# Kernel optimization log

Hardware: AMD Instinct MI355X
Metric: run time of the kernel (lower is better)

Reference implementation:

```python
import jax, jax.numpy as jnp
import numpy as np

B, T, NE = 2, 2048, 1024
NH, NKV, HD = 16, 4, 64
GC = 32  # ve_gate_channels
WIN = 1024  # sliding window (left)
EPS = 1e-6


def rope(x, cos, sin):
    # x: (B,T,H,D), cos/sin: (B,T,D//2)
    cos = cos[:, :, None, :]
    sin = sin[:, :, None, :]
    x1, x2 = jnp.split(x, 2, axis=-1)
    return jnp.concatenate([x1 * cos + x2 * sin, -x1 * sin + x2 * cos], axis=-1)


def rmsnorm(x):
    return x * jax.lax.rsqrt(jnp.mean(x * x, axis=-1, keepdims=True) + EPS)


def setup_inputs() -> dict:
    key = jax.random.key(0)
    ks = jax.random.split(key, 7)
    x = jax.random.normal(ks[0], (B, T, NE), jnp.float32)
    ve = jax.random.normal(ks[1], (B, T, NKV * HD), jnp.float32)
    # real RoPE tables (already 'sliced to correct positions')
    inv_freq = 1.0 / (10000.0 ** (jnp.arange(HD // 2, dtype=jnp.float32) / (HD // 2)))
    ang = jnp.arange(T, dtype=jnp.float32)[:, None] * inv_freq[None, :]  # (T, D//2)
    cos = jnp.broadcast_to(jnp.cos(ang)[None], (B, T, HD // 2))
    sin = jnp.broadcast_to(jnp.sin(ang)[None], (B, T, HD // 2))
    s = 0.02
    Wq = jax.random.normal(ks[2], (NE, NH * HD), jnp.float32) * s
    Wk = jax.random.normal(ks[3], (NE, NKV * HD), jnp.float32) * s
    Wv = jax.random.normal(ks[4], (NE, NKV * HD), jnp.float32) * s
    Wo = jax.random.normal(ks[5], (NE, NE), jnp.float32) * s
    Wg = jax.random.normal(ks[6], (GC, NKV), jnp.float32) * s
    return {"x": x, "ve": ve, "cos": cos, "sin": sin,
            "Wq": Wq, "Wk": Wk, "Wv": Wv, "Wo": Wo, "Wg": Wg,
            "window_size": WIN}


def reference(x, ve, cos, sin, Wq, Wk, Wv, Wo, Wg, window_size):
    Bs, Ts, _ = x.shape
    q = (x @ Wq).reshape(Bs, Ts, NH, HD)
    k = (x @ Wk).reshape(Bs, Ts, NKV, HD)
    v = (x @ Wv).reshape(Bs, Ts, NKV, HD)
    # gated value embeddings
    gate = 2.0 * jax.nn.sigmoid(x[..., :GC] @ Wg)  # (B,T,NKV)
    v = v + gate[..., None] * ve.reshape(Bs, Ts, NKV, HD)
    q = rmsnorm(rope(q, cos, sin))
    k = rmsnorm(rope(k, cos, sin))
    # GQA: head h uses kv head h // rep
    rep = NH // NKV
    k = jnp.repeat(k, rep, axis=2)
    v = jnp.repeat(v, rep, axis=2)
    scale = 1.0 / jnp.sqrt(jnp.float32(HD))
    scores = jnp.einsum('bthd,bshd->bhts', q, k) * scale  # (B,H,T,T)
    i = jnp.arange(Ts)[:, None]
    j = jnp.arange(Ts)[None, :]
    mask = (j <= i) & (i - j <= window_size)  # causal + sliding window
    scores = jnp.where(mask, scores, -jnp.inf)
    p = jax.nn.softmax(scores, axis=-1)
    y = jnp.einsum('bhts,bshd->bthd', p, v).reshape(Bs, Ts, NE)
    return y @ Wo
```

## Files before the change

kernel.cpp:

```cpp
#include <hip/hip_runtime.h>
#include <hip/hip_bf16.h>
#include <string.h>

typedef __attribute__((ext_vector_type(8))) short bf16x8;
typedef __attribute__((ext_vector_type(4))) short bf16x4;
typedef __attribute__((ext_vector_type(4))) float f32x4;
typedef __attribute__((ext_vector_type(4))) int i32x4;
typedef __attribute__((ext_vector_type(2))) int i32x2;

#define DEV __device__ __forceinline__
#define WIN_ 1024

DEV short f2bf(float f) {
  __hip_bfloat16 h = __float2bfloat16(f);
  short s; __builtin_memcpy(&s, &h, 2); return s;
}
DEV float bf2f(short s) {
  union { unsigned u; float f; } a; a.u = ((unsigned)(unsigned short)s) << 16;
  return a.f;
}
DEV unsigned pkbf2(float a, float b) {
  __hip_bfloat162 h = __float22bfloat162_rn(make_float2(a, b));
  unsigned u; __builtin_memcpy(&u, &h, 4); return u;
}
DEV float fexp2(float x) {
#if __has_builtin(__builtin_amdgcn_exp2f)
  return __builtin_amdgcn_exp2f(x);
#else
  return exp2f(x);
#endif
}

DEV f32x4 mfma16(bf16x4 a, bf16x4 b, f32x4 c) {
#if __has_builtin(__builtin_amdgcn_mfma_f32_16x16x16bf16_1k)
  return __builtin_amdgcn_mfma_f32_16x16x16bf16_1k(a, b, c, 0, 0, 0);
#else
  asm volatile("s_nop 1\n\tv_mfma_f32_16x16x16_bf16 %0, %1, %2, %0\n\ts_nop 7\n\ts_nop 7"
               : "+v"(c) : "v"(a), "v"(b));
  return c;
#endif
}

DEV void gload16(const short* g, short* l) {
  __builtin_amdgcn_global_load_lds((const __attribute__((address_space(1))) unsigned int*)g,
                                   (__attribute__((address_space(3))) unsigned int*)l,
                                   16, 0, 0);
}

__global__ __launch_bounds__(256) void k_prep(const float* __restrict__ x,
    const float* __restrict__ Wq, const float* __restrict__ Wk, const float* __restrict__ Wv,
    const float* __restrict__ Wo, short* __restrict__ xb, short* __restrict__ WbT,
    short* __restrict__ WoT) {
  const int bid = blockIdx.x;
  if (bid < 4096) {
    int i = bid * 256 + threadIdx.x;
    f32x4 v = *(const f32x4*)(x + (size_t)i * 4);
    i32x2 o = {(int)pkbf2(v[0], v[1]), (int)pkbf2(v[2], v[3])};
    *(i32x2*)(xb + (size_t)i * 4) = o;
    return;
  }
  int t = bid - 4096;
  const float* src; short* dst; int srcld, bx, by;
  if (t < 1024)      { src = Wq; dst = WbT;                        srcld = 1024; bx = t & 31;          by = t >> 5; }
  else if (t < 1280) { src = Wk; dst = WbT + (size_t)1024 * 1024;  srcld = 256;  bx = (t - 1024) & 7;  by = (t - 1024) >> 3; }
  else if (t < 1536) { src = Wv; dst = WbT + (size_t)1280 * 1024;  srcld = 256;  bx = (t - 1280) & 7;  by = (t - 1280) >> 3; }
  else               { src = Wo; dst = WoT;                        srcld = 1024; bx = (t - 1536) & 31; by = (t - 1536) >> 5; }
  __shared__ float tile[32][33];
  const int n0 = bx * 32, k0 = by * 32;
  const int tx = threadIdx.x & 31, ty = threadIdx.x >> 5;
#pragma unroll
  for (int i = 0; i < 4; ++i)
    tile[ty * 4 + i][tx] = src[(size_t)(k0 + ty * 4 + i) * srcld + n0 + tx];
  __syncthreads();
#pragma unroll
  for (int i = 0; i < 4; ++i)
    dst[(size_t)(n0 + ty * 4 + i) * 1024 + k0 + tx] = f2bf(tile[tx][ty * 4 + i]);
}

__global__ __launch_bounds__(256) void k_gemm_qkv(const short* __restrict__ A, const short* __restrict__ BT,
    const float* __restrict__ x, const float* __restrict__ ve,
    const float* __restrict__ cosp, const float* __restrict__ sinp, const float* __restrict__ Wg,
    short* __restrict__ qh, short* __restrict__ kh, short* __restrict__ vhT) {
  const int K = 1024;
  __shared__ short As[2][8192];
  __shared__ short Bs[2][4096];
  const int tid = threadIdx.x;
  const int l = tid & 63, w = tid >> 6;
  const int l15 = l & 15, hi = l >> 4;
  const int bx = blockIdx.x;
  const int m0 = blockIdx.y * 128, n0 = bx * 64;
  const int srow = tid >> 3;
  const int segsw = 8 * ((tid & 7) ^ (srow & 7));
  const int lo = tid * 8;
  const short* pa = A + (size_t)(m0 + srow) * K + segsw;
  const short* pb = BT + (size_t)(n0 + srow) * K + segsw;
  const int f8 = l15 & 7;

  f32x4 acc[2][4];
#pragma unroll
  for (int i = 0; i < 2; ++i)
#pragma unroll
    for (int j = 0; j < 4; ++j) acc[i][j] = (f32x4){0.f, 0.f, 0.f, 0.f};

  auto stage = [&](int buf, int koff) {
    gload16(pa + koff,          &As[buf][lo]);
    gload16(pa + 32 * K + koff, &As[buf][lo + 2048]);
    gload16(pa + 64 * K + koff, &As[buf][lo + 4096]);
    gload16(pa + 96 * K + koff, &As[buf][lo + 6144]);
    gload16(pb + koff,          &Bs[buf][lo]);
    gload16(pb + 32 * K + koff, &Bs[buf][lo + 2048]);
  };

  stage(0, 0);
  __syncthreads();
  int cur = 0;
  for (int k0 = 0; k0 < K; k0 += 64) {
    if (k0 + 64 < K) stage(cur ^ 1, k0 + 64);
    bf16x8 af[2][2], bfr[4][2];
#pragma unroll
    for (int c = 0; c < 2; ++c) {
      int seg = 8 * ((4 * c + hi) ^ f8);
#pragma unroll
      for (int mi = 0; mi < 2; ++mi)
        af[mi][c] = *(const bf16x8*)&As[cur][(32 * w + 16 * mi + l15) * 64 + seg];
#pragma unroll
      for (int ni = 0; ni < 4; ++ni)
        bfr[ni][c] = *(const bf16x8*)&Bs[cur][(16 * ni + l15) * 64 + seg];
    }
#pragma unroll
    for (int c = 0; c < 2; ++c)
#pragma unroll
      for (int mi = 0; mi < 2; ++mi)
#pragma unroll
        for (int ni = 0; ni < 4; ++ni)
          acc[mi][ni] = __builtin_amdgcn_mfma_f32_16x16x32_bf16(af[mi][c], bfr[ni][c], acc[mi][ni], 0, 0, 0);
    __syncthreads();
    cur ^= 1;
  }

  if (bx < 20) {
    short* dst0 = (bx < 16) ? qh : kh;
#pragma unroll
    for (int mi = 0; mi < 2; ++mi)
#pragma unroll
      for (int r = 0; r < 4; ++r) {
        int bt = m0 + 32 * w + 16 * mi + 4 * hi + r;
        int b = bt >> 11, t = bt & 2047;
        float c0 = cosp[bt * 32 + l15],      s0 = sinp[bt * 32 + l15];
        float c1 = cosp[bt * 32 + 16 + l15], s1 = sinp[bt * 32 + 16 + l15];
        float a0 = acc[mi][0][r], b0 = acc[mi][2][r];
        float a1 = acc[mi][1][r], b1 = acc[mi][3][r];
        float o0 = a0 * c0 + b0 * s0;
        float o2 = b0 * c0 - a0 * s0;
        float o1 = a1 * c1 + b1 * s1;
        float o3 = b1 * c1 - a1 * s1;
        float ss = o0 * o0 + o1 * o1 + o2 * o2 + o3 * o3;
        ss += __shfl_xor(ss, 1); ss += __shfl_xor(ss, 2);
        ss += __shfl_xor(ss, 4); ss += __shfl_xor(ss, 8);
        float rinv = rsqrtf(ss * (1.f / 64.f) + 1e-6f);
        if (bx < 16) rinv *= 0.18033688011112042f;
        size_t rb = ((size_t)((b * ((bx < 16) ? 16 : 4) + ((bx < 16) ? bx : bx - 16)) * 2048 + t)) * 64;
        dst0[rb + l15]      = f2bf(o0 * rinv);
        dst0[rb + 16 + l15] = f2bf(o1 * rinv);
        dst0[rb + 32 + l15] = f2bf(o2 * rinv);
        dst0[rb + 48 + l15] = f2bf(o3 * rinv);
      }
  } else {
    const int kvh = bx - 20;
#pragma unroll
    for (int mi = 0; mi < 2; ++mi)
#pragma unroll
      for (int r = 0; r < 4; ++r) {
        int bt = m0 + 32 * w + 16 * mi + 4 * hi + r;
        int b = bt >> 11, t = bt & 2047;
        const float* xr = x + (size_t)bt * 1024;
        float z = 0.f;
#pragma unroll
        for (int gg = 0; gg < 32; ++gg) z += xr[gg] * Wg[gg * 4 + kvh];
        float gate = 2.f / (1.f + __expf(-z));
        const float* vep = ve + (size_t)bt * 256 + kvh * 64;
        short* dst = vhT + (size_t)(b * 4 + kvh) * 131072 + t;
#pragma unroll
        for (int ni = 0; ni < 4; ++ni) {
          int d = 16 * ni + l15;
          float vv = acc[mi][ni][r] + gate * vep[d];
          dst[(size_t)d * 2048] = f2bf(vv);
        }
      }
  }
}

template <int LDC, bool F32OUT>
__global__ __launch_bounds__(256) void k_gemm_bt(const short* __restrict__ A, const short* __restrict__ BT,
                                                 void* __restrict__ Cv, int K) {
  __shared__ short As[2][8192];
  __shared__ short Bs[2][4096];
  const int tid = threadIdx.x;
  const int l = tid & 63, w = tid >> 6;
  const int l15 = l & 15, hi = l >> 4;
  const int m0 = blockIdx.y * 128, n0 = blockIdx.x * 64;
  const int srow = tid >> 3;
  const int segsw = 8 * ((tid & 7) ^ (srow & 7));
  const int lo = tid * 8;
  const short* pa = A + (size_t)(m0 + srow) * K + segsw;
  const short* pb = BT + (size_t)(n0 + srow) * K + segsw;
  const int f8 = l15 & 7;

  f32x4 acc[2][4];
#pragma unroll
  for (int i = 0; i < 2; ++i)
#pragma unroll
    for (int j = 0; j < 4; ++j) acc[i][j] = (f32x4){0.f, 0.f, 0.f, 0.f};

  auto stage = [&](int buf, int koff) {
    gload16(pa + koff,          &As[buf][lo]);
    gload16(pa + 32 * K + koff, &As[buf][lo + 2048]);
    gload16(pa + 64 * K + koff, &As[buf][lo + 4096]);
    gload16(pa + 96 * K + koff, &As[buf][lo + 6144]);
    gload16(pb + koff,          &Bs[buf][lo]);
    gload16(pb + 32 * K + koff, &Bs[buf][lo + 2048]);
  };

  stage(0, 0);
  __syncthreads();
  int cur = 0;
  for (int k0 = 0; k0 < K; k0 += 64) {
    if (k0 + 64 < K) stage(cur ^ 1, k0 + 64);
    bf16x8 af[2][2], bfr[4][2];
#pragma unroll
    for (int c = 0; c < 2; ++c) {
      int seg = 8 * ((4 * c + hi) ^ f8);
#pragma unroll
      for (int mi = 0; mi < 2; ++mi)
        af[mi][c] = *(const bf16x8*)&As[cur][(32 * w + 16 * mi + l15) * 64 + seg];
#pragma unroll
      for (int ni = 0; ni < 4; ++ni)
        bfr[ni][c] = *(const bf16x8*)&Bs[cur][(16 * ni + l15) * 64 + seg];
    }
#pragma unroll
    for (int c = 0; c < 2; ++c)
#pragma unroll
      for (int mi = 0; mi < 2; ++mi)
#pragma unroll
        for (int ni = 0; ni < 4; ++ni)
          acc[mi][ni] = __builtin_amdgcn_mfma_f32_16x16x32_bf16(af[mi][c], bfr[ni][c], acc[mi][ni], 0, 0, 0);
    __syncthreads();
    cur ^= 1;
  }
#pragma unroll
  for (int mi = 0; mi < 2; ++mi)
#pragma unroll
    for (int ni = 0; ni < 4; ++ni)
#pragma unroll
      for (int r = 0; r < 4; ++r) {
        int crow = m0 + 32 * w + 16 * mi + 4 * hi + r;
        int ccol = n0 + 16 * ni + l15;
        if (F32OUT) ((float*)Cv)[(size_t)crow * LDC + ccol] = acc[mi][ni][r];
        else        ((short*)Cv)[(size_t)crow * LDC + ccol] = f2bf(acc[mi][ni][r]);
      }
}

__global__ __launch_bounds__(256) void k_attn(const short* __restrict__ qh, const short* __restrict__ kh,
                                              const short* __restrict__ vhT, short* __restrict__ yb) {
  __shared__ i32x4 lds4[2][1024];
  char* base = (char*)lds4;
  const int bid = blockIdx.x;
  const int kq = bid >> 8, low = bid & 255;
  const int h = low & 15, b = (low >> 4) & 1, q0 = low >> 5;
  const int qt = (kq == 0) ? (31 - q0) : (kq == 1) ? (16 + q0) : (kq == 2) ? (15 - q0) : q0;
  const int kvh = h >> 2;
  const int qs = qt * 64;
  const int tid = threadIdx.x;
  const int w = tid >> 6, l = tid & 63, l15 = l & 15, hi = l >> 4;
  const int qi = qs + 16 * w + l15;
  const int rsw = (l15 & 7) << 4;

  const short* qb = qh + ((size_t)((b * 16 + h) * 2048 + qs + 16 * w + l15)) * 64;
  bf16x8 qf0 = *(const bf16x8*)(qb + 8 * hi);
  bf16x8 qf1 = *(const bf16x8*)(qb + 32 + 8 * hi);

  f32x4 oacc[4];
#pragma unroll
  for (int i = 0; i < 4; ++i) oacc[i] = (f32x4){0.f, 0.f, 0.f, 0.f};
  float lsum = 0.f;

  const int kt_lo = (qs >= 1024) ? ((qs - 1024) >> 6) : 0;
  const int kt_hi = qs >> 6;
  const short* kbase = kh + ((size_t)(b * 4 + kvh) * 2048) * 64;
  const short* vbase = vhT + ((size_t)(b * 4 + kvh) * 64) * 2048;

  const int srow = tid >> 3, sseg = tid & 7;
  const int swz = (srow & 7) << 4;
  const int ko = ((srow << 7) + (sseg << 4)) ^ swz;
  const short* kp = kbase + (size_t)(kt_lo * 64 + srow) * 64 + sseg * 8;
  const short* vp = vbase + (size_t)srow * 2048 + kt_lo * 64 + sseg * 8;
  i32x4 rk0, rk1, rv0, rv1;

#define LOADT() do { \
    rk0 = *(const i32x4*)kp; \
    rk1 = *(const i32x4*)(kp + 2048); \
    rv0 = *(const i32x4*)vp; \
    rv1 = *(const i32x4*)(vp + 32 * 2048); \
  } while (0)

#define WRITET(DST) do { \
    char* kd = (DST); \
    *(i32x4*)(kd + ko) = rk0; \
    *(i32x4*)(kd + ko + 4096) = rk1; \
    char* vd = kd + 8192; \
    *(i32x4*)(vd + ko) = rv0; \
    *(i32x4*)(vd + ko + 4096) = rv1; \
  } while (0)

  auto TILE = [&](char* kbuf, int kt) {
    char* vbuf = kbuf + 8192;
    f32x4 s[4];
#pragma unroll
    for (int nt = 0; nt < 4; ++nt) s[nt] = (f32x4){0.f, 0.f, 0.f, 0.f};
#pragma unroll
    for (int c = 0; c < 2; ++c) {
      bf16x8 qc = c ? qf1 : qf0;
#pragma unroll
      for (int nt = 0; nt < 4; ++nt) {
        bf16x8 kf = *(const bf16x8*)(kbuf + ((((16 * nt + l15) << 7) + (c << 6) + (hi << 4)) ^ rsw));
        s[nt] = __builtin_amdgcn_mfma_f32_16x16x32_bf16(kf, qc, s[nt], 0, 0, 0);
      }
    }
    if (kt == kt_lo || kt == kt_hi) {
      const int k0 = kt * 64;
#pragma unroll
      for (int nt = 0; nt < 4; ++nt)
#pragma unroll
        for (int r = 0; r < 4; ++r) {
          int kj = k0 + 16 * nt + 4 * hi + r;
          if (kj > qi || (qi - kj) > WIN_) s[nt][r] = -1e30f;
        }
    }
#pragma unroll
    for (int nt = 0; nt < 4; ++nt)
#pragma unroll
      for (int r = 0; r < 4; ++r) s[nt][r] = fexp2(fminf(s[nt][r], 12.5f));
    float r0 = (s[0][0] + s[0][1]) + (s[0][2] + s[0][3]);
    float r1 = (s[1][0] + s[1][1]) + (s[1][2] + s[1][3]);
    float r2 = (s[2][0] + s[2][1]) + (s[2][2] + s[2][3]);
    float r3 = (s[3][0] + s[3][1]) + (s[3][2] + s[3][3]);
    lsum += (r0 + r1) + (r2 + r3);

    bf16x4 pa[4];
#pragma unroll
    for (int nt = 0; nt < 4; ++nt) {
      i32x2 pk = {(int)pkbf2(s[nt][0], s[nt][1]), (int)pkbf2(s[nt][2], s[nt][3])};
      pa[nt] = __builtin_bit_cast(bf16x4, pk);
    }
#pragma unroll
    for (int dt = 0; dt < 4; ++dt) {
      int rowb = ((16 * dt + l15) << 7) + (hi << 3);
#pragma unroll
      for (int nt = 0; nt < 4; ++nt) {
        i32x2 vv = *(const i32x2*)(vbuf + ((rowb + 32 * nt) ^ rsw));
        oacc[dt] = mfma16(__builtin_bit_cast(bf16x4, vv), pa[nt], oacc[dt]);
      }
    }
  };

  LOADT();
  WRITET(base);
  __syncthreads();

  int kt = kt_lo;
  for (;;) {
    if (kt < kt_hi) { kp += 4096; vp += 64; LOADT(); }
    __builtin_amdgcn_s_setprio(1);
    TILE(base, kt);
    __builtin_amdgcn_s_setprio(0);
    if (kt < kt_hi) WRITET(base + 16384);
    __syncthreads();
    if (kt == kt_hi) break;
    ++kt;
    if (kt < kt_hi) { kp += 4096; vp += 64; LOADT(); }
    __builtin_amdgcn_s_setprio(1);
    TILE(base + 16384, kt);
    __builtin_amdgcn_s_setprio(0);
    if (kt < kt_hi) WRITET(base);
    __syncthreads();
    if (kt == kt_hi) break;
    ++kt;
  }
#undef LOADT
#undef WRITET

  lsum += __shfl_xor(lsum, 16);
  lsum += __shfl_xor(lsum, 32);

  float inv = 1.f / lsum;
  size_t orow = (size_t)(b * 2048 + qs + 16 * w + l15);
#pragma unroll
  for (int dt = 0; dt < 4; ++dt) {
    int col0 = h * 64 + 16 * dt + 4 * hi;
    i32x2 pk = {(int)pkbf2(oacc[dt][0] * inv, oacc[dt][1] * inv),
                (int)pkbf2(oacc[dt][2] * inv, oacc[dt][3] * inv)};
    *(i32x2*)(yb + orow * 1024 + col0) = pk;
  }
}

extern "C" void kernel_launch(void* const* d_in, const int* in_sizes, int n_in,
                              void* d_out, int out_size, void* d_ws, size_t ws_size,
                              hipStream_t stream) {
  const float* x    = (const float*)d_in[0];
  const float* ve   = (const float*)d_in[1];
  const float* cosp = (const float*)d_in[2];
  const float* sinp = (const float*)d_in[3];
  const float* Wq   = (const float*)d_in[4];
  const float* Wk   = (const float*)d_in[5];
  const float* Wv   = (const float*)d_in[6];
  const float* Wo   = (const float*)d_in[7];
  const float* Wg   = (const float*)d_in[8];
  float* out = (float*)d_out;

  char* ws = (char*)d_ws;
  short* xb   = (short*)(ws);
  short* WbT  = (short*)(ws + 8388608);
  short* WoT  = (short*)(ws + 11534336);
  short* qh   = (short*)(ws + 26214400);
  short* kh   = (short*)(ws + 34603008);
  short* vhT  = (short*)(ws + 36700160);
  short* yb   = (short*)(ws + 38797312);

  k_prep<<<6656, 256, 0, stream>>>(x, Wq, Wk, Wv, Wo, xb, WbT, WoT);

  k_gemm_qkv<<<dim3(24, 32), 256, 0, stream>>>(xb, WbT, x, ve, cosp, sinp, Wg, qh, kh, vhT);

  k_attn<<<1024, 256, 0, stream>>>(qh, kh, vhT, yb);

  k_gemm_bt<1024, true><<<dim3(16, 32), 256, 0, stream>>>(yb, WoT, out, 1024);
}
```

Baseline: 85.77 us.

## Fuse x fp32-to-bf16 conversion into QKV GEMM A-tile staging; narrow attn setprio

The separate pass converting x to bf16 in the prep kernel is removed. The QKV GEMM now loads fp32 x directly into registers, packs it to bf16, and writes it to LDS after the MFMA loop, with prefetching done through registers instead of async global-to-LDS copies. This drops one full write and read of the bf16 copy of x and shrinks the prep launch. The cost is that each GEMM block rereads fp32 x, doing twice the A bytes per tile across 24 column blocks, and uses more registers. Attention setprio regions are also narrowed to cover only the MFMA sections.

```diff
diff --git a/kernel.cpp b/kernel.cpp
--- a/kernel.cpp
+++ b/kernel.cpp
@@ -47,19 +47,10 @@
                                    16, 0, 0);
 }
 
-__global__ __launch_bounds__(256) void k_prep(const float* __restrict__ x,
-    const float* __restrict__ Wq, const float* __restrict__ Wk, const float* __restrict__ Wv,
-    const float* __restrict__ Wo, short* __restrict__ xb, short* __restrict__ WbT,
-    short* __restrict__ WoT) {
-  const int bid = blockIdx.x;
-  if (bid < 4096) {
-    int i = bid * 256 + threadIdx.x;
-    f32x4 v = *(const f32x4*)(x + (size_t)i * 4);
-    i32x2 o = {(int)pkbf2(v[0], v[1]), (int)pkbf2(v[2], v[3])};
-    *(i32x2*)(xb + (size_t)i * 4) = o;
-    return;
-  }
-  int t = bid - 4096;
+__global__ __launch_bounds__(256) void k_prep(const float* __restrict__ Wq, const float* __restrict__ Wk,
+    const float* __restrict__ Wv, const float* __restrict__ Wo,
+    short* __restrict__ WbT, short* __restrict__ WoT) {
+  int t = blockIdx.x;
   const float* src; short* dst; int srcld, bx, by;
   if (t < 1024)      { src = Wq; dst = WbT;                        srcld = 1024; bx = t & 31;          by = t >> 5; }
   else if (t < 1280) { src = Wk; dst = WbT + (size_t)1024 * 1024;  srcld = 256;  bx = (t - 1024) & 7;  by = (t - 1024) >> 3; }
@@ -77,7 +68,7 @@
     dst[(size_t)(n0 + ty * 4 + i) * 1024 + k0 + tx] = f2bf(tile[tx][ty * 4 + i]);
 }
 
-__global__ __launch_bounds__(256) void k_gemm_qkv(const short* __restrict__ A, const short* __restrict__ BT,
+__global__ __launch_bounds__(256) void k_gemm_qkv(const short* __restrict__ BT,
     const float* __restrict__ x, const float* __restrict__ ve,
     const float* __restrict__ cosp, const float* __restrict__ sinp, const float* __restrict__ Wg,
     short* __restrict__ qh, short* __restrict__ kh, short* __restrict__ vhT) {
@@ -92,7 +83,7 @@
   const int srow = tid >> 3;
   const int segsw = 8 * ((tid & 7) ^ (srow & 7));
   const int lo = tid * 8;
-  const short* pa = A + (size_t)(m0 + srow) * K + segsw;
+  const float* pxa = x + (size_t)(m0 + srow) * 1024 + segsw;
   const short* pb = BT + (size_t)(n0 + srow) * K + segsw;
   const int f8 = l15 & 7;
 
@@ -102,20 +93,37 @@
 #pragma unroll
     for (int j = 0; j < 4; ++j) acc[i][j] = (f32x4){0.f, 0.f, 0.f, 0.f};
 
-  auto stage = [&](int buf, int koff) {
-    gload16(pa + koff,          &As[buf][lo]);
-    gload16(pa + 32 * K + koff, &As[buf][lo + 2048]);
-    gload16(pa + 64 * K + koff, &As[buf][lo + 4096]);
-    gload16(pa + 96 * K + koff, &As[buf][lo + 6144]);
+  f32x4 u[8];
+  auto stage_load = [&](int koff) {
+#pragma unroll
+    for (int ch = 0; ch < 4; ++ch) {
+      const float* p = pxa + (size_t)ch * 32768 + koff;
+      u[2 * ch]     = *(const f32x4*)p;
+      u[2 * ch + 1] = *(const f32x4*)(p + 4);
+    }
+  };
+  auto stage_write = [&](int buf) {
+#pragma unroll
+    for (int ch = 0; ch < 4; ++ch) {
+      i32x4 pk = {(int)pkbf2(u[2 * ch][0], u[2 * ch][1]),
+                  (int)pkbf2(u[2 * ch][2], u[2 * ch][3]),
+                  (int)pkbf2(u[2 * ch + 1][0], u[2 * ch + 1][1]),
+                  (int)pkbf2(u[2 * ch + 1][2], u[2 * ch + 1][3])};
+      *(i32x4*)&As[buf][lo + ch * 2048] = pk;
+    }
+  };
+  auto stage_b = [&](int buf, int koff) {
     gload16(pb + koff,          &Bs[buf][lo]);
     gload16(pb + 32 * K + koff, &Bs[buf][lo + 2048]);
   };
 
-  stage(0, 0);
+  stage_load(0);
+  stage_b(0, 0);
+  stage_write(0);
   __syncthreads();
   int cur = 0;
   for (int k0 = 0; k0 < K; k0 += 64) {
-    if (k0 + 64 < K) stage(cur ^ 1, k0 + 64);
+    if (k0 + 64 < K) { stage_load(k0 + 64); stage_b(cur ^ 1, k0 + 64); }
     bf16x8 af[2][2], bfr[4][2];
 #pragma unroll
     for (int c = 0; c < 2; ++c) {
@@ -134,6 +142,7 @@
 #pragma unroll
         for (int ni = 0; ni < 4; ++ni)
           acc[mi][ni] = __builtin_amdgcn_mfma_f32_16x16x32_bf16(af[mi][c], bfr[ni][c], acc[mi][ni], 0, 0, 0);
+    if (k0 + 64 < K) stage_write(cur ^ 1);
     __syncthreads();
     cur ^= 1;
   }
@@ -317,6 +326,7 @@
     f32x4 s[4];
 #pragma unroll
     for (int nt = 0; nt < 4; ++nt) s[nt] = (f32x4){0.f, 0.f, 0.f, 0.f};
+    __builtin_amdgcn_s_setprio(1);
 #pragma unroll
     for (int c = 0; c < 2; ++c) {
       bf16x8 qc = c ? qf1 : qf0;
@@ -326,6 +336,7 @@
         s[nt] = __builtin_amdgcn_mfma_f32_16x16x32_bf16(kf, qc, s[nt], 0, 0, 0);
       }
     }
+    __builtin_amdgcn_s_setprio(0);
     if (kt == kt_lo || kt == kt_hi) {
       const int k0 = kt * 64;
 #pragma unroll
@@ -352,6 +363,7 @@
       i32x2 pk = {(int)pkbf2(s[nt][0], s[nt][1]), (int)pkbf2(s[nt][2], s[nt][3])};
       pa[nt] = __builtin_bit_cast(bf16x4, pk);
     }
+    __builtin_amdgcn_s_setprio(1);
 #pragma unroll
     for (int dt = 0; dt < 4; ++dt) {
       int rowb = ((16 * dt + l15) << 7) + (hi << 3);
@@ -361,6 +373,7 @@
         oacc[dt] = mfma16(__builtin_bit_cast(bf16x4, vv), pa[nt], oacc[dt]);
       }
     }
+    __builtin_amdgcn_s_setprio(0);
   };
 
   LOADT();
@@ -370,17 +383,13 @@
   int kt = kt_lo;
   for (;;) {
     if (kt < kt_hi) { kp += 4096; vp += 64; LOADT(); }
-    __builtin_amdgcn_s_setprio(1);
     TILE(base, kt);
-    __builtin_amdgcn_s_setprio(0);
     if (kt < kt_hi) WRITET(base + 16384);
     __syncthreads();
     if (kt == kt_hi) break;
     ++kt;
     if (kt < kt_hi) { kp += 4096; vp += 64; LOADT(); }
-    __builtin_amdgcn_s_setprio(1);
     TILE(base + 16384, kt);
-    __builtin_amdgcn_s_setprio(0);
     if (kt < kt_hi) WRITET(base);
     __syncthreads();
     if (kt == kt_hi) break;
@@ -418,7 +427,6 @@
   float* out = (float*)d_out;
 
   char* ws = (char*)d_ws;
-  short* xb   = (short*)(ws);
   short* WbT  = (short*)(ws + 8388608);
   short* WoT  = (short*)(ws + 11534336);
   short* qh   = (short*)(ws + 26214400);
@@ -426,9 +434,9 @@
   short* vhT  = (short*)(ws + 36700160);
   short* yb   = (short*)(ws + 38797312);
 
-  k_prep<<<6656, 256, 0, stream>>>(x, Wq, Wk, Wv, Wo, xb, WbT, WoT);
-
-  k_gemm_qkv<<<dim3(24, 32), 256, 0, stream>>>(xb, WbT, x, ve, cosp, sinp, Wg, qh, kh, vhT);
+  k_prep<<<2560, 256, 0, stream>>>(Wq, Wk, Wv, Wo, WbT, WoT);
+
+  k_gemm_qkv<<<dim3(24, 32), 256, 0, stream>>>(WbT, x, ve, cosp, sinp, Wg, qh, kh, vhT);
 
   k_attn<<<1024, 256, 0, stream>>>(qh, kh, vhT, yb);
 
```

Result: slower. 97.36 us (+13.5%).
